# Kernel optimization log

Measured on AMD Instinct MI355X. Metric: run time of the kernel, lower is better.

Reference implementation:

```python
import jax, jax.numpy as jnp
import numpy as np

GMAX = 1.0   # args.gmax
GMIN = 0.01  # args.gmin
EPS = 0.1    # args.e_train


def setup_inputs() -> dict:
    key = jax.random.key(0)
    k1, k2, k3, k4 = jax.random.split(key, 4)
    N, B, NIN, NOUT, E = 8, 32, 128, 128, 1024
    # analog signals live in [0, 1]
    a_previous = jax.random.uniform(k1, (N, B, NIN, E), dtype=jnp.float32)
    # conductance params (clamped to [-gmax, gmax] in forward)
    theta = jax.random.uniform(k2, (NIN + 2, NOUT), dtype=jnp.float32) * 2.0 - 1.0
    # per-replica multiplicative noise seed in [0, 1); forward maps to 1 +- eps
    noise = jax.random.uniform(k3, (N, NIN + 2, NOUT), dtype=jnp.float32)
    # printed-tanh activation params eta = [offset, scale, shift, slope]
    eta = jnp.array([0.0, 1.0, 0.0, 1.0], dtype=jnp.float32) + 0.1 * jax.random.normal(k4, (4,), dtype=jnp.float32)
    return {"a_previous": a_previous, "theta": theta, "noise": noise, "eta": eta}


def reference(a_previous, theta, noise, eta):
    sg = jax.lax.stop_gradient
    # theta property: clamp + gmin pruning with straight-through estimator
    t = jnp.clip(theta, -GMAX, GMAX)
    t = jnp.where(jnp.abs(t) < GMIN, 0.0, t)
    theta_eff = sg(t) + theta - sg(theta)
    # theta_noisy: replicate over N with multiplicative uniform noise in [1-eps, 1+eps]
    theta_noisy = theta_eff[None, :, :] * ((noise * 2.0 - 1.0) * EPS + 1.0)  # [N, M, O], M = n_in+2
    # W: abs-normalized conductances per output column group
    abs_tn = jnp.abs(theta_noisy)
    W = abs_tn / (jnp.sum(abs_tn, axis=1, keepdims=True) + 1e-10)
    # sign masks (constants w.r.t. grad: values fully overwritten in torch)
    pos = sg((theta_noisy >= 0.0).astype(theta_noisy.dtype))
    neg = 1.0 - pos
    # a: [N, B, n_in, E] -> [N, B, E, n_in]; append ones and zeros columns
    a_r = jnp.transpose(a_previous, (0, 1, 3, 2))
    ones = jnp.ones(a_r.shape[:3] + (1,), a_r.dtype)
    zeros = jnp.zeros_like(ones)
    a_ext = jnp.concatenate([a_r, ones, zeros], axis=3)  # [N, B, E, M]
    # INV: unipolar complement; zero the last (zeros) column after inversion
    a_neg = (1.0 - a_ext).at[..., -1].set(0.0)
    # split-sign MAC: z [N, B, E, n_out]
    z = (jnp.einsum('nbem,nmo->nbeo', a_ext, W * pos)
         + jnp.einsum('nbem,nmo->nbeo', a_neg, W * neg))
    # printed tanh activation
    act = eta[0] + eta[1] * jnp.tanh((z - eta[2]) * eta[3])
    # back to [N, B, n_out, E]
    return jnp.transpose(act, (0, 1, 3, 2))
```

## Files before the change

### kernel.cpp

```cpp
#include <hip/hip_runtime.h>
#include <hip/hip_bf16.h>
#include <stdint.h>

#define N_REP 8
#define BATCH 32
#define NIN   128
#define NOUT  128
#define EDIM  1024
#define MDIM  130
#define ETILE 128
#define SE    130

typedef __attribute__((ext_vector_type(8))) short short8;
typedef __attribute__((ext_vector_type(4))) float f32x4;

__device__ __forceinline__ unsigned short f2bf(float f) {
    union { float f; uint32_t u; } v;
    v.f = f;
    uint32_t u = v.u;
    uint32_t r = u + 0x7fffu + ((u >> 16) & 1u);
    return (unsigned short)(r >> 16);
}

__device__ __forceinline__ uint32_t pk2bf(float lo, float hi) {
    __hip_bfloat162 h = __float22bfloat162_rn(make_float2(lo, hi));
    uint32_t d;
    __builtin_memcpy(&d, &h, 4);
    return d;
}

__global__ __launch_bounds__(64)
void prep_kernel(const float* __restrict__ theta,
                 const float* __restrict__ noise,
                 unsigned short* __restrict__ Sg,
                 float* __restrict__ biasg) {
    const int n = blockIdx.x >> 7;
    const int o = blockIdx.x & 127;
    const int lane = threadIdx.x;

    const float* nb = noise + (size_t)n * MDIM * NOUT + o;
    auto tn_at = [&](int m) -> float {
        float t = theta[m * NOUT + o];
        t = fminf(fmaxf(t, -1.f), 1.f);
        if (fabsf(t) < 0.01f) t = 0.f;
        return t * fmaf(nb[m * NOUT], 0.2f, 0.9f);
    };

    const float t0 = tn_at(lane);
    const float t1 = tn_at(lane + 64);
    const float t2 = (lane < 2) ? tn_at(128 + lane) : 0.f;

    float s = fabsf(t0) + fabsf(t1) + fabsf(t2);
#pragma unroll
    for (int d = 1; d < 64; d <<= 1) s += __shfl_xor(s, d, 64);
    const float inv = 1.f / (s + 1e-10f);

    const float w0 = fabsf(t0) * inv, w1 = fabsf(t1) * inv;
    unsigned short* srow = Sg + ((size_t)n * NOUT + o) * NIN;
    srow[lane]      = f2bf(t0 >= 0.f ? w0 : -w0);
    srow[lane + 64] = f2bf(t1 >= 0.f ? w1 : -w1);

    float b = (t0 < 0.f ? w0 : 0.f) + (t1 < 0.f ? w1 : 0.f);
    if (lane == 0 && t2 >= 0.f) b += fabsf(t2) * inv;
#pragma unroll
    for (int d = 1; d < 64; d <<= 1) b += __shfl_xor(b, d, 64);
    if (lane == 0) biasg[n * NOUT + o] = b;
}

__global__ __launch_bounds__(256, 4)
void gemm_kernel(const float* __restrict__ a,
                 const unsigned short* __restrict__ Sg,
                 const float* __restrict__ biasg,
                 const float* __restrict__ eta,
                 float* __restrict__ out) {
    __shared__ uint32_t Alds[64 * SE];
    const int bid = blockIdx.x;
    const int et  = bid & 7;
    const int nb  = bid >> 3;
    const int n   = nb >> 5;
    const int tid = threadIdx.x;

    {
        const float* abase = a + (size_t)nb * (NIN * EDIM) + et * ETILE;
        const int e4  = (tid & 31) << 2;
        const int mp0 = tid >> 5;
#pragma unroll
        for (int it = 0; it < 8; ++it) {
            const int mp = mp0 + (it << 3);
            const float4 va = *(const float4*)(abase + (size_t)(2 * mp) * EDIM + e4);
            const float4 vb = *(const float4*)(abase + (size_t)(2 * mp + 1) * EDIM + e4);
            uint2 d0, d1;
            d0.x = pk2bf(va.x, vb.x);
            d0.y = pk2bf(va.y, vb.y);
            d1.x = pk2bf(va.z, vb.z);
            d1.y = pk2bf(va.w, vb.w);
            *(uint2*)&Alds[mp * SE + e4]     = d0;
            *(uint2*)&Alds[mp * SE + e4 + 2] = d1;
        }
    }
    __syncthreads();

    const int lane = tid & 63;
    const int w = tid >> 6;
    const int r = lane & 15;
    const int q = lane >> 4;
    const int o_base = (w & 1) << 6;
    const int e_base = (w >> 1) << 6;

    f32x4 acc[4][4];
#pragma unroll
    for (int fo = 0; fo < 4; ++fo)
#pragma unroll
        for (int fe = 0; fe < 4; ++fe)
            acc[fo][fe] = (f32x4){0.f, 0.f, 0.f, 0.f};

#pragma unroll
    for (int ks = 0; ks < 4; ++ks) {
        short8 sf[4];
#pragma unroll
        for (int fo = 0; fo < 4; ++fo) {
            const int o = o_base + (fo << 4) + r;
            sf[fo] = *(const short8*)(Sg + ((size_t)(n * NOUT + o) << 7) + (ks << 5) + (q << 3));
        }
        short8 af[4];
        const int mpb = (ks << 4) + (q << 2);
#pragma unroll
        for (int fe = 0; fe < 4; ++fe) {
            const int e = e_base + (fe << 4) + r;
            uint32_t d[4];
#pragma unroll
            for (int jj = 0; jj < 4; ++jj)
                d[jj] = Alds[(mpb + jj) * SE + e];
            __builtin_memcpy(&af[fe], d, 16);
        }
#pragma unroll
        for (int fo = 0; fo < 4; ++fo)
#pragma unroll
            for (int fe = 0; fe < 4; ++fe)
                acc[fo][fe] = __builtin_amdgcn_mfma_f32_16x16x32_bf16(
                    sf[fo], af[fe], acc[fo][fe], 0, 0, 0);
    }

    const float e0 = eta[0], e1 = eta[1], e2 = eta[2], e3 = eta[3];
    float* obase = out + (size_t)nb * (NOUT * EDIM) + et * ETILE;
#pragma unroll
    for (int fo = 0; fo < 4; ++fo) {
        const int orow0 = o_base + (fo << 4) + (q << 2);
        const float4 bias4 = *(const float4*)(biasg + n * NOUT + orow0);
        const float bv[4] = {bias4.x, bias4.y, bias4.z, bias4.w};
#pragma unroll
        for (int i = 0; i < 4; ++i) {
            float* orow = obase + (size_t)(orow0 + i) * EDIM;
#pragma unroll
            for (int fe = 0; fe < 4; ++fe) {
                const float z = acc[fo][fe][i] + bv[i];
                const float y = (z - e2) * e3;
                const float ex = __expf(2.f * y);
                const float th = 1.f - 2.f * __builtin_amdgcn_rcpf(ex + 1.f);
                orow[e_base + (fe << 4) + r] = fmaf(e1, th, e0);
            }
        }
    }
}

extern "C" void kernel_launch(void* const* d_in, const int* in_sizes, int n_in,
                              void* d_out, int out_size, void* d_ws, size_t ws_size,
                              hipStream_t stream) {
    const float* a     = (const float*)d_in[0];
    const float* theta = (const float*)d_in[1];
    const float* noise = (const float*)d_in[2];
    const float* eta   = (const float*)d_in[3];
    float* out = (float*)d_out;

    unsigned short* Sg = (unsigned short*)d_ws;
    float* biasg = (float*)((char*)d_ws + (size_t)N_REP * NOUT * NIN * sizeof(unsigned short));

    prep_kernel<<<N_REP * NOUT, 64, 0, stream>>>(theta, noise, Sg, biasg);
    gemm_kernel<<<N_REP * BATCH * (EDIM / ETILE), 256, 0, stream>>>(a, Sg, biasg, eta, out);
}
```

Measured before the change: 254.6 us.

## Make gemm blocks persistent over four E-tiles with double-buffered LDS prefetch

Each block now handles four consecutive 128-wide E tiles instead of one. Global loads of the next activation tile are issued into registers and converted to bf16 into a second LDS buffer while the current tile's MFMAs run. The S weight fragments and bias are loaded once per block and reused across tiles. The MFMA operands are swapped so each lane writes float4-contiguous output, and the tanh is folded into exp2 with precomputed constants. The cost is fewer blocks (512), higher register and LDS use, and occupancy lowered to 2 blocks per SIMD in the launch bounds.

```diff
diff --git a/kernel.cpp b/kernel.cpp
--- a/kernel.cpp
+++ b/kernel.cpp
@@ -10,6 +10,7 @@
 #define MDIM  130
 #define ETILE 128
 #define SE    130
+#define TILES 4
 
 typedef __attribute__((ext_vector_type(8))) short short8;
 typedef __attribute__((ext_vector_type(4))) float f32x4;
@@ -67,39 +68,18 @@
     if (lane == 0) biasg[n * NOUT + o] = b;
 }
 
-__global__ __launch_bounds__(256, 4)
+__global__ __launch_bounds__(256, 2)
 void gemm_kernel(const float* __restrict__ a,
                  const unsigned short* __restrict__ Sg,
                  const float* __restrict__ biasg,
                  const float* __restrict__ eta,
                  float* __restrict__ out) {
-    __shared__ uint32_t Alds[64 * SE];
+    __shared__ uint32_t Alds[2][64 * SE];
     const int bid = blockIdx.x;
-    const int et  = bid & 7;
-    const int nb  = bid >> 3;
+    const int nb  = bid >> 1;
+    const int eh  = bid & 1;
     const int n   = nb >> 5;
     const int tid = threadIdx.x;
-
-    {
-        const float* abase = a + (size_t)nb * (NIN * EDIM) + et * ETILE;
-        const int e4  = (tid & 31) << 2;
-        const int mp0 = tid >> 5;
-#pragma unroll
-        for (int it = 0; it < 8; ++it) {
-            const int mp = mp0 + (it << 3);
-            const float4 va = *(const float4*)(abase + (size_t)(2 * mp) * EDIM + e4);
-            const float4 vb = *(const float4*)(abase + (size_t)(2 * mp + 1) * EDIM + e4);
-            uint2 d0, d1;
-            d0.x = pk2bf(va.x, vb.x);
-            d0.y = pk2bf(va.y, vb.y);
-            d1.x = pk2bf(va.z, vb.z);
-            d1.y = pk2bf(va.w, vb.w);
-            *(uint2*)&Alds[mp * SE + e4]     = d0;
-            *(uint2*)&Alds[mp * SE + e4 + 2] = d1;
-        }
-    }
-    __syncthreads();
-
     const int lane = tid & 63;
     const int w = tid >> 6;
     const int r = lane & 15;
@@ -107,57 +87,114 @@
     const int o_base = (w & 1) << 6;
     const int e_base = (w >> 1) << 6;
 
-    f32x4 acc[4][4];
-#pragma unroll
-    for (int fo = 0; fo < 4; ++fo)
-#pragma unroll
-        for (int fe = 0; fe < 4; ++fe)
-            acc[fo][fe] = (f32x4){0.f, 0.f, 0.f, 0.f};
-
-#pragma unroll
-    for (int ks = 0; ks < 4; ++ks) {
-        short8 sf[4];
+    short8 sf[4][4];
+#pragma unroll
+    for (int ks = 0; ks < 4; ++ks)
 #pragma unroll
         for (int fo = 0; fo < 4; ++fo) {
             const int o = o_base + (fo << 4) + r;
-            sf[fo] = *(const short8*)(Sg + ((size_t)(n * NOUT + o) << 7) + (ks << 5) + (q << 3));
-        }
-        short8 af[4];
-        const int mpb = (ks << 4) + (q << 2);
-#pragma unroll
-        for (int fe = 0; fe < 4; ++fe) {
-            const int e = e_base + (fe << 4) + r;
-            uint32_t d[4];
-#pragma unroll
-            for (int jj = 0; jj < 4; ++jj)
-                d[jj] = Alds[(mpb + jj) * SE + e];
-            __builtin_memcpy(&af[fe], d, 16);
-        }
-#pragma unroll
-        for (int fo = 0; fo < 4; ++fo)
+            sf[ks][fo] = *(const short8*)(Sg + ((size_t)(n * NOUT + o) << 7) + (ks << 5) + (q << 3));
+        }
+    float bv[4];
+#pragma unroll
+    for (int fo = 0; fo < 4; ++fo)
+        bv[fo] = biasg[n * NOUT + o_base + (fo << 4) + r];
+    const float kk = eta[3] * 2.885390082f;
+    const float kd = -eta[2] * kk;
+    const float kA = eta[0] + eta[1];
+    const float kB = 2.f * eta[1];
+
+    const float* abase0 = a   + (size_t)nb * (NIN  * EDIM) + (size_t)(eh << 2) * ETILE;
+    float*       obase0 = out + (size_t)nb * (NOUT * EDIM) + (size_t)(eh << 2) * ETILE;
+
+    const int e4  = (tid & 31) << 2;
+    const int mp0 = tid >> 5;
+
+    float4 pf[8];
+    auto issue = [&](int t, int half) {
+        const float* ab = abase0 + t * ETILE;
+#pragma unroll
+        for (int it = 0; it < 4; ++it) {
+            const int mp = mp0 + (it << 3) + (half << 5);
+            pf[2 * it]     = *(const float4*)(ab + (size_t)(2 * mp)     * EDIM + e4);
+            pf[2 * it + 1] = *(const float4*)(ab + (size_t)(2 * mp + 1) * EDIM + e4);
+        }
+    };
+    auto commit = [&](int buf, int half) {
+#pragma unroll
+        for (int it = 0; it < 4; ++it) {
+            const int mp = mp0 + (it << 3) + (half << 5);
+            uint2 d0, d1;
+            d0.x = pk2bf(pf[2 * it].x, pf[2 * it + 1].x);
+            d0.y = pk2bf(pf[2 * it].y, pf[2 * it + 1].y);
+            d1.x = pk2bf(pf[2 * it].z, pf[2 * it + 1].z);
+            d1.y = pk2bf(pf[2 * it].w, pf[2 * it + 1].w);
+            *(uint2*)&Alds[buf][mp * SE + e4]     = d0;
+            *(uint2*)&Alds[buf][mp * SE + e4 + 2] = d1;
+        }
+    };
+
+    issue(0, 0); commit(0, 0);
+    issue(0, 1); commit(0, 1);
+    __syncthreads();
+
+    for (int t = 0; t < TILES; ++t) {
+        const int cur = t & 1;
+
+        if (t < TILES - 1) issue(t + 1, 0);
+
+        f32x4 acc[4][4];
+#pragma unroll
+        for (int fe = 0; fe < 4; ++fe)
+#pragma unroll
+            for (int fo = 0; fo < 4; ++fo)
+                acc[fe][fo] = (f32x4){0.f, 0.f, 0.f, 0.f};
+
+#pragma unroll
+        for (int ks = 0; ks < 4; ++ks) {
+            if (ks == 2 && t < TILES - 1) {
+                commit(cur ^ 1, 0);
+                issue(t + 1, 1);
+            }
+            short8 af[4];
+            const int mpb = (ks << 4) + (q << 2);
+#pragma unroll
+            for (int fe = 0; fe < 4; ++fe) {
+                const int e = e_base + (fe << 4) + r;
+                uint32_t d[4];
+#pragma unroll
+                for (int jj = 0; jj < 4; ++jj)
+                    d[jj] = Alds[cur][(mpb + jj) * SE + e];
+                __builtin_memcpy(&af[fe], d, 16);
+            }
 #pragma unroll
             for (int fe = 0; fe < 4; ++fe)
-                acc[fo][fe] = __builtin_amdgcn_mfma_f32_16x16x32_bf16(
-                    sf[fo], af[fe], acc[fo][fe], 0, 0, 0);
-    }
-
-    const float e0 = eta[0], e1 = eta[1], e2 = eta[2], e3 = eta[3];
-    float* obase = out + (size_t)nb * (NOUT * EDIM) + et * ETILE;
-#pragma unroll
-    for (int fo = 0; fo < 4; ++fo) {
-        const int orow0 = o_base + (fo << 4) + (q << 2);
-        const float4 bias4 = *(const float4*)(biasg + n * NOUT + orow0);
-        const float bv[4] = {bias4.x, bias4.y, bias4.z, bias4.w};
-#pragma unroll
-        for (int i = 0; i < 4; ++i) {
-            float* orow = obase + (size_t)(orow0 + i) * EDIM;
+#pragma unroll
+                for (int fo = 0; fo < 4; ++fo)
+                    acc[fe][fo] = __builtin_amdgcn_mfma_f32_16x16x32_bf16(
+                        af[fe], sf[ks][fo], acc[fe][fo], 0, 0, 0);
+        }
+
+        if (t < TILES - 1) {
+            commit(cur ^ 1, 1);
+            __syncthreads();
+        }
+
+        float* obase = obase0 + t * ETILE;
+#pragma unroll
+        for (int fo = 0; fo < 4; ++fo) {
+            const int o = o_base + (fo << 4) + r;
+            float* orow = obase + (size_t)o * EDIM;
 #pragma unroll
             for (int fe = 0; fe < 4; ++fe) {
-                const float z = acc[fo][fe][i] + bv[i];
-                const float y = (z - e2) * e3;
-                const float ex = __expf(2.f * y);
-                const float th = 1.f - 2.f * __builtin_amdgcn_rcpf(ex + 1.f);
-                orow[e_base + (fe << 4) + r] = fmaf(e1, th, e0);
+                float vv[4];
+#pragma unroll
+                for (int i = 0; i < 4; ++i) {
+                    const float z  = acc[fe][fo][i] + bv[fo];
+                    const float ex = __builtin_amdgcn_exp2f(fmaf(z, kk, kd));
+                    vv[i] = fmaf(-kB, __builtin_amdgcn_rcpf(ex + 1.f), kA);
+                }
+                *(float4*)(orow + e_base + (fe << 4) + (q << 2)) = *(float4*)vv;
             }
         }
     }
@@ -176,5 +213,5 @@
     float* biasg = (float*)((char*)d_ws + (size_t)N_REP * NOUT * NIN * sizeof(unsigned short));
 
     prep_kernel<<<N_REP * NOUT, 64, 0, stream>>>(theta, noise, Sg, biasg);
-    gemm_kernel<<<N_REP * BATCH * (EDIM / ETILE), 256, 0, stream>>>(a, Sg, biasg, eta, out);
-}
+    gemm_kernel<<<N_REP * BATCH * 2, 256, 0, stream>>>(a, Sg, biasg, eta, out);
+}
```

Measured after the change: 261.4 us. 1.03x slower.
